# Optimization experiments

Measured on AMD Instinct MI355X. Metric: run time of the kernel, lower is better.

## Reference

```python
import jax, jax.numpy as jnp
import numpy as np

DIM = 512
EPS = 1e-8
LN_EPS = 1e-5


def _layernorm(x, g, b):
    mu = jnp.mean(x, axis=-1, keepdims=True)
    var = jnp.mean(jnp.square(x - mu), axis=-1, keepdims=True)
    return (x - mu) * jax.lax.rsqrt(var + LN_EPS) * g + b


def setup_inputs() -> dict:
    key = jax.random.key(0)
    ks = jax.random.split(key, 8)
    b, i, j, d = 8, 2048, 2048, DIM
    s = 1.0 / np.sqrt(d)
    return {
        "inputs": jax.random.normal(ks[0], (b, i, d), dtype=jnp.float32),
        "context": jax.random.normal(ks[1], (b, j, d), dtype=jnp.float32),
        "g_in": jnp.ones((d,), jnp.float32),
        "b_in": jnp.zeros((d,), jnp.float32),
        "g_ctx": jnp.ones((d,), jnp.float32),
        "b_ctx": jnp.zeros((d,), jnp.float32),
        "Wq": jax.random.uniform(ks[2], (d, d), jnp.float32, -s, s),
        "bq": jnp.zeros((d,), jnp.float32),
        "Wk": jax.random.uniform(ks[3], (d, d), jnp.float32, -s, s),
        "bk": jnp.zeros((d,), jnp.float32),
        "Wv": jax.random.uniform(ks[4], (d, d), jnp.float32, -s, s),
        "bv": jnp.zeros((d,), jnp.float32),
    }


def reference(inputs, context, g_in, b_in, g_ctx, b_ctx, Wq, bq, Wk, bk, Wv, bv):
    scale = DIM ** (-0.5)
    x = _layernorm(inputs, g_in, b_in)
    c = _layernorm(context, g_ctx, b_ctx)
    q = x @ Wq + bq          # [b,i,d]
    k = c @ Wk + bk          # [b,j,d]
    v = c @ Wv + bv          # [b,j,d]
    dots = jnp.einsum('bid,bjd->bij', q, k) * scale
    # NOTE: non-standard softmax over the QUERY axis (dim=1), then eps shift
    attn = jax.nn.softmax(dots, axis=1) + EPS
    # second renormalization over the KEY axis (dim=2)
    mean_attn = attn / (jnp.sum(attn, axis=2, keepdims=True) + EPS)
    updates = jnp.einsum('bjd,bij->bid', v, mean_attn)
    return updates
```

## Files before the change

kernel.cpp:

```cpp
#include <hip/hip_runtime.h>
#include <hip/hip_bf16.h>
#include <math.h>

#define EPSF 1e-8f
#define LN_EPSF 1e-5f
#define SCALE_QK 0.04419417382415922f

typedef unsigned short ushort_t;
typedef __bf16 bhalf;
typedef bhalf bhalf8 __attribute__((ext_vector_type(8)));
typedef float f32x4 __attribute__((ext_vector_type(4)));

__device__ __forceinline__ float b2f(ushort_t u) {
    return __uint_as_float((unsigned)u << 16);
}
__device__ __forceinline__ ushort_t f2b(float f) {
    unsigned x = __float_as_uint(f);
    return (ushort_t)((x + 0x7fffu + ((x >> 16) & 1u)) >> 16);
}
__device__ __forceinline__ unsigned pk2(float lo, float hi) {
    return (unsigned)f2b(lo) | ((unsigned)f2b(hi) << 16);
}
__device__ __forceinline__ void gload16(const ushort_t* g, ushort_t* l) {
    __builtin_amdgcn_global_load_lds(
        (const __attribute__((address_space(1))) unsigned int*)g,
        (__attribute__((address_space(3))) unsigned int*)l, 16, 0, 0);
}

__global__ __launch_bounds__(256) void mv_bias_kernel(
    const float* __restrict__ Wq, const float* __restrict__ Wk,
    const float* __restrict__ bq, const float* __restrict__ bk,
    float* __restrict__ wqbk, float* __restrict__ wkbq, float* __restrict__ cc)
{
    __shared__ float ls[4];
    const int y = blockIdx.y;
    const int t = threadIdx.x;
    if (y == 2) {
        if (blockIdx.x != 0) return;
        float s = bq[t] * bk[t] + bq[t + 256] * bk[t + 256];
#pragma unroll
        for (int off = 32; off > 0; off >>= 1) s += __shfl_down(s, off, 64);
        int lane = t & 63, w = t >> 6;
        if (lane == 0) ls[w] = s;
        __syncthreads();
        if (t == 0) cc[0] = ls[0] + ls[1] + ls[2] + ls[3];
        return;
    }
    const float* W = y ? Wk : Wq;
    const float* v = y ? bq : bk;
    float* o = y ? wkbq : wqbk;
    const int row = blockIdx.x * 16 + (t >> 4);
    const int l = t & 15;
    const float* wr = W + (size_t)row * 512 + l * 32;
    const float* vr = v + l * 32;
    float s = 0.f;
#pragma unroll
    for (int c = 0; c < 32; ++c) s += wr[c] * vr[c];
#pragma unroll
    for (int off = 8; off > 0; off >>= 1) s += __shfl_down(s, off, 16);
    if (l == 0) o[row] = s;
}

__global__ __launch_bounds__(256) void ln_apply_kernel(
    const float* __restrict__ X1, const float* __restrict__ X2,
    const float* __restrict__ g1, const float* __restrict__ b1,
    const float* __restrict__ g2, const float* __restrict__ b2,
    const float* __restrict__ wb1, const float* __restrict__ wb2,
    ushort_t* __restrict__ O1, ushort_t* __restrict__ O2,
    float* __restrict__ T1, float* __restrict__ T2)
{
    const bool sec = blockIdx.y != 0;
    const float* X = sec ? X2 : X1;
    const float* g = sec ? g2 : g1;
    const float* b = sec ? b2 : b1;
    const float* wb = sec ? wb2 : wb1;
    ushort_t* O = sec ? O2 : O1;
    float* T = sec ? T2 : T1;
    const size_t base = (size_t)blockIdx.x * 512;
    const int t = threadIdx.x;
    float2 x = ((const float2*)(X + base))[t];
    float s = x.x + x.y;
    float q = fmaf(x.x, x.x, x.y * x.y);
#pragma unroll
    for (int off = 32; off > 0; off >>= 1) {
        s += __shfl_down(s, off, 64);
        q += __shfl_down(q, off, 64);
    }
    __shared__ float ls[4], lq[4], mv[2], ld[4];
    int lane = t & 63, w = t >> 6;
    if (lane == 0) { ls[w] = s; lq[w] = q; }
    __syncthreads();
    if (t == 0) {
        float st = ls[0] + ls[1] + ls[2] + ls[3];
        float qt = lq[0] + lq[1] + lq[2] + lq[3];
        float mu = st * (1.0f / 512.0f);
        float var = qt * (1.0f / 512.0f) - mu * mu;
        mv[0] = mu;
        mv[1] = rsqrtf(var + LN_EPSF);
    }
    __syncthreads();
    const float mu = mv[0], rstd = mv[1];
    float2 gg = ((const float2*)g)[t];
    float2 bb = ((const float2*)b)[t];
    float2 ww = ((const float2*)wb)[t];
    float o0 = (x.x - mu) * rstd * gg.x + bb.x;
    float o1 = (x.y - mu) * rstd * gg.y + bb.y;
    ((unsigned*)O)[blockIdx.x * 256 + t] = pk2(o0, o1);
    float d = o0 * ww.x + o1 * ww.y;
#pragma unroll
    for (int off = 32; off > 0; off >>= 1) d += __shfl_down(d, off, 64);
    if (lane == 0) ld[w] = d;
    __syncthreads();
    if (t == 0) T[blockIdx.x] = ld[0] + ld[1] + ld[2] + ld[3];
}

__global__ __launch_bounds__(256) void wprep_kernel(
    const float* __restrict__ Wq, const float* __restrict__ Wk,
    const float* __restrict__ Wv,
    ushort_t* __restrict__ Wqb, ushort_t* __restrict__ Wkb,
    ushort_t* __restrict__ WvT)
{
    const int z = blockIdx.z;
    if (z < 2) {
        const float* W = z ? Wk : Wq;
        ushort_t* T = z ? Wkb : Wqb;
        size_t idx = ((size_t)(blockIdx.y * 16 + blockIdx.x)) * 1024 + threadIdx.x * 4;
        float4 f = *(const float4*)(W + idx);
        uint2 u;
        u.x = pk2(f.x, f.y);
        u.y = pk2(f.z, f.w);
        *(uint2*)(T + idx) = u;
        return;
    }
    __shared__ float tile[32][33];
    int tx = threadIdx.x & 31, ty = threadIdx.x >> 5;
    int r0 = blockIdx.y * 32, c0 = blockIdx.x * 32;
#pragma unroll
    for (int p = 0; p < 4; ++p)
        tile[ty + p * 8][tx] = Wv[(size_t)(r0 + ty + p * 8) * 512 + c0 + tx];
    __syncthreads();
#pragma unroll
    for (int p = 0; p < 4; ++p)
        WvT[(size_t)(c0 + ty + p * 8) * 512 + r0 + tx] = f2b(tile[tx][ty + p * 8]);
}

__global__ __launch_bounds__(256) void colrecip_kernel(
    const float* __restrict__ cs, float* __restrict__ cr,
    ushort_t* __restrict__ crs)
{
    int t = blockIdx.x * 256 + threadIdx.x;
    float r = 1.0f / cs[t];
    cr[t] = r;
    crs[t] = f2b(r);
}

template <int MODE>
__global__ __launch_bounds__(256) void mfma_gemm_kernel(
    const ushort_t* __restrict__ A, const ushort_t* __restrict__ B,
    void* __restrict__ Cout,
    const float* __restrict__ bias,
    const float* __restrict__ t1,
    const float* __restrict__ t2,
    const float* __restrict__ cc,
    float* __restrict__ colsum,
    const float* __restrict__ crcol,
    const ushort_t* __restrict__ crs,
    int K, int N, size_t strideA, size_t strideB, size_t strideC,
    float scale)
{
    __shared__ __align__(16) ushort_t As[128 * 64];
    __shared__ __align__(16) ushort_t Bs[128 * 64];
    __shared__ __align__(16) ushort_t crs_lds[(MODE == 2) ? 2048 : 8];
    const int tid = threadIdx.x;
    const ushort_t* Ab = A + strideA * blockIdx.z;
    const ushort_t* Bb = B + strideB * blockIdx.z;
    const int m0 = blockIdx.y * 128;
    const int n0 = blockIdx.x * 128;
    const int wave = tid >> 6;
    const int lane = tid & 63;
    const int fm = lane & 15;
    const int fq = lane >> 4;
    const int fq4 = fq * 4;
    const int fm7 = fm & 7;
    const int wm = (wave >> 1) * 64;
    const int wn = (wave & 1) * 64;

    const int lrow = lane >> 3;
    const int lchunk = lane & 7;
    const int scs = lchunk ^ lrow;

    const ushort_t* aSrc[4]; const ushort_t* bSrc[4];
    ushort_t* aDst[4]; ushort_t* bDst[4];
#pragma unroll
    for (int p = 0; p < 4; ++p) {
        int row = wave * 32 + p * 8 + lrow;
        aSrc[p] = Ab + (size_t)(m0 + row) * K + scs * 8;
        bSrc[p] = Bb + (size_t)(n0 + row) * K + scs * 8;
        aDst[p] = As + (wave * 32 + p * 8) * 64 + lane * 8;
        bDst[p] = Bs + (wave * 32 + p * 8) * 64 + lane * 8;
    }

    if (MODE == 2) {
        uint4 c4 = *(const uint4*)(crs + (size_t)blockIdx.z * 2048 + tid * 8);
        *(uint4*)&crs_lds[tid * 8] = c4;
    }

    const int cBase = fq ^ fm7;
    const ushort_t* aFrag[4]; const ushort_t* bFrag[4];
#pragma unroll
    for (int t = 0; t < 4; ++t) {
        aFrag[t] = As + (wm + t * 16 + fm) * 64;
        bFrag[t] = Bs + (wn + t * 16 + fm) * 64;
    }

    f32x4 acc[4][4];
    f32x4 sacc[4];
#pragma unroll
    for (int i = 0; i < 4; ++i) {
        sacc[i] = (f32x4){0.f, 0.f, 0.f, 0.f};
#pragma unroll
        for (int j = 0; j < 4; ++j) acc[i][j] = (f32x4){0.f, 0.f, 0.f, 0.f};
    }

    for (int k0 = 0; k0 < K; k0 += 64) {
        __syncthreads();
#pragma unroll
        for (int p = 0; p < 4; ++p) {
            gload16(aSrc[p] + k0, aDst[p]);
            gload16(bSrc[p] + k0, bDst[p]);
        }
        __syncthreads();
#pragma unroll
        for (int s = 0; s < 2; ++s) {
            const int off = ((cBase ^ (s << 2)) << 3);
            bhalf8 af[4], bf[4];
#pragma unroll
            for (int t = 0; t < 4; ++t) {
                af[t] = *(const bhalf8*)(aFrag[t] + off);
                bf[t] = *(const bhalf8*)(bFrag[t] + off);
            }
#pragma unroll
            for (int i = 0; i < 4; ++i)
#pragma unroll
                for (int j = 0; j < 4; ++j)
                    acc[i][j] = __builtin_amdgcn_mfma_f32_16x16x32_bf16(
                        bf[j], af[i], acc[i][j], 0, 0, 0);
            if (MODE == 2) {
                bhalf8 bc = *(const bhalf8*)&crs_lds[k0 + (s << 5) + (fq << 3)];
#pragma unroll
                for (int i = 0; i < 4; ++i)
                    sacc[i] = __builtin_amdgcn_mfma_f32_16x16x32_bf16(
                        bc, af[i], sacc[i], 0, 0, 0);
            }
        }
    }

    if (MODE == 2) {
        float* C = (float*)Cout + strideC * blockIdx.z;
#pragma unroll
        for (int ti = 0; ti < 4; ++ti) {
            const int row = m0 + wm + ti * 16 + fm;
            const float rs = 1.0f / (sacc[ti][0] + 2.049e-5f);
            float* Cr = C + (size_t)row * N + n0 + wn + fq4;
#pragma unroll
            for (int tj = 0; tj < 4; ++tj) {
                f32x4 v;
#pragma unroll
                for (int r = 0; r < 4; ++r) v[r] = acc[ti][tj][r] * rs;
                *(f32x4*)(Cr + tj * 16) = v;
            }
        }
    } else if (MODE == 1) {
        ushort_t* C = (ushort_t*)Cout + strideC * blockIdx.z;
        const float cv = cc[0];
        f32x4 t2c[4];
#pragma unroll
        for (int tj = 0; tj < 4; ++tj) {
            float4 tv = *(const float4*)(t2 + (size_t)blockIdx.z * 2048 +
                                         n0 + wn + tj * 16 + fq4);
            t2c[tj][0] = tv.x + cv;
            t2c[tj][1] = tv.y + cv;
            t2c[tj][2] = tv.z + cv;
            t2c[tj][3] = tv.w + cv;
        }
        float psum[4][4];
#pragma unroll
        for (int tj = 0; tj < 4; ++tj)
#pragma unroll
            for (int r = 0; r < 4; ++r) psum[tj][r] = 0.f;
#pragma unroll
        for (int ti = 0; ti < 4; ++ti) {
            const int row = m0 + wm + ti * 16 + fm;
            const float t1v = t1[(size_t)blockIdx.z * 2048 + row];
            ushort_t* Cr = C + (size_t)row * N + n0 + wn + fq4;
#pragma unroll
            for (int tj = 0; tj < 4; ++tj) {
                ushort_t h0 = f2b(__expf((acc[ti][tj][0] + t1v + t2c[tj][0]) * scale));
                ushort_t h1 = f2b(__expf((acc[ti][tj][1] + t1v + t2c[tj][1]) * scale));
                ushort_t h2 = f2b(__expf((acc[ti][tj][2] + t1v + t2c[tj][2]) * scale));
                ushort_t h3 = f2b(__expf((acc[ti][tj][3] + t1v + t2c[tj][3]) * scale));
                uint2 u;
                u.x = (unsigned)h0 | ((unsigned)h1 << 16);
                u.y = (unsigned)h2 | ((unsigned)h3 << 16);
                *(uint2*)(Cr + tj * 16) = u;
                psum[tj][0] += b2f(h0);
                psum[tj][1] += b2f(h1);
                psum[tj][2] += b2f(h2);
                psum[tj][3] += b2f(h3);
            }
        }
#pragma unroll
        for (int tj = 0; tj < 4; ++tj)
#pragma unroll
            for (int r = 0; r < 4; ++r) {
                float v = psum[tj][r];
                v += __shfl_xor(v, 1, 64);
                v += __shfl_xor(v, 2, 64);
                v += __shfl_xor(v, 4, 64);
                v += __shfl_xor(v, 8, 64);
                psum[tj][r] = v;
            }
        float* colpart = (float*)&As[0];
        __syncthreads();
        if (tid < 128) colpart[tid] = 0.f;
        __syncthreads();
        if (fm == 0) {
#pragma unroll
            for (int tj = 0; tj < 4; ++tj)
#pragma unroll
                for (int r = 0; r < 4; ++r)
                    atomicAdd(&colpart[wn + tj * 16 + fq4 + r], psum[tj][r]);
        }
        __syncthreads();
        if (tid < 128)
            atomicAdd(&colsum[(size_t)blockIdx.z * 2048 + n0 + tid], colpart[tid]);
    } else if (MODE == 3) {
        ushort_t* C = (ushort_t*)Cout + strideC * blockIdx.z;
        f32x4 crv[4];
#pragma unroll
        for (int tj = 0; tj < 4; ++tj) {
            float4 cq = *(const float4*)(crcol + (size_t)blockIdx.z * 2048 +
                                         n0 + wn + tj * 16 + fq4);
            crv[tj][0] = cq.x; crv[tj][1] = cq.y;
            crv[tj][2] = cq.z; crv[tj][3] = cq.w;
        }
#pragma unroll
        for (int ti = 0; ti < 4; ++ti) {
            const int row = m0 + wm + ti * 16 + fm;
            const float bvv = bias[row];
            ushort_t* Cr = C + (size_t)row * N + n0 + wn + fq4;
#pragma unroll
            for (int tj = 0; tj < 4; ++tj) {
                uint2 u;
                u.x = pk2((acc[ti][tj][0] + bvv) * crv[tj][0],
                          (acc[ti][tj][1] + bvv) * crv[tj][1]);
                u.y = pk2((acc[ti][tj][2] + bvv) * crv[tj][2],
                          (acc[ti][tj][3] + bvv) * crv[tj][3]);
                *(uint2*)(Cr + tj * 16) = u;
            }
        }
    } else {
        ushort_t* C = (ushort_t*)Cout + strideC * blockIdx.z;
#pragma unroll
        for (int ti = 0; ti < 4; ++ti) {
            const int row = m0 + wm + ti * 16 + fm;
            ushort_t* Cr = C + (size_t)row * N + n0 + wn + fq4;
#pragma unroll
            for (int tj = 0; tj < 4; ++tj) {
                uint2 u;
                u.x = pk2(acc[ti][tj][0], acc[ti][tj][1]);
                u.y = pk2(acc[ti][tj][2], acc[ti][tj][3]);
                *(uint2*)(Cr + tj * 16) = u;
            }
        }
    }
}

extern "C" void kernel_launch(void* const* d_in, const int* in_sizes, int n_in,
                              void* d_out, int out_size, void* d_ws, size_t ws_size,
                              hipStream_t stream)
{
    const float* inputs  = (const float*)d_in[0];
    const float* context = (const float*)d_in[1];
    const float* g_in    = (const float*)d_in[2];
    const float* b_in    = (const float*)d_in[3];
    const float* g_ctx   = (const float*)d_in[4];
    const float* b_ctx   = (const float*)d_in[5];
    const float* Wq      = (const float*)d_in[6];
    const float* bq      = (const float*)d_in[7];
    const float* Wk      = (const float*)d_in[8];
    const float* bk      = (const float*)d_in[9];
    const float* Wv      = (const float*)d_in[10];
    const float* bv      = (const float*)d_in[11];
    float* out = (float*)d_out;

    const size_t QKV  = 8ull * 2048 * 512;
    const size_t WSZ  = 512ull * 512;
    const size_t DOTS = 8ull * 2048 * 2048;

    ushort_t* xln   = (ushort_t*)d_ws;
    ushort_t* cln   = xln + QKV;
    ushort_t* Wqb   = cln + QKV;
    ushort_t* Wkb   = Wqb + WSZ;
    ushort_t* WvT   = Wkb + WSZ;
    ushort_t* Mb    = WvT + WSZ;
    ushort_t* KM    = Mb + WSZ;
    ushort_t* vTs   = KM + QKV;
    ushort_t* edots = vTs + QKV;
    ushort_t* crs   = edots + DOTS;
    float* fbase    = (float*)(crs + 16384);
    float* colsum   = fbase;
    float* colrecip = colsum + 16384;
    float* t1       = colrecip + 16384;
    float* t2       = t1 + 16384;
    float* wqbk     = t2 + 16384;
    float* wkbq     = wqbk + 512;
    float* cc       = wkbq + 512;
    size_t need_bytes = (4 * QKV + 4 * WSZ + DOTS + 16384) * 2
                      + (4 * 16384 + 1024 + 1) * 4;
    if (ws_size < need_bytes) return;

    hipMemsetAsync(colsum, 0, 16384 * sizeof(float), stream);

    mv_bias_kernel<<<dim3(32, 3), 256, 0, stream>>>(Wq, Wk, bq, bk, wqbk, wkbq, cc);

    ln_apply_kernel<<<dim3(16384, 2), 256, 0, stream>>>(
        inputs, context, g_in, b_in, g_ctx, b_ctx, wqbk, wkbq, xln, cln, t1, t2);

    wprep_kernel<<<dim3(16, 16, 3), 256, 0, stream>>>(Wq, Wk, Wv, Wqb, Wkb, WvT);

    mfma_gemm_kernel<0><<<dim3(4, 4, 1), 256, 0, stream>>>(
        Wqb, Wkb, Mb, nullptr, nullptr, nullptr, nullptr, nullptr, nullptr, nullptr,
        512, 512, 0, 0, 0, 1.f);

    mfma_gemm_kernel<0><<<dim3(4, 128, 1), 256, 0, stream>>>(
        cln, Mb, KM, nullptr, nullptr, nullptr, nullptr, nullptr, nullptr, nullptr,
        512, 512, 0, 0, 0, 1.f);

    mfma_gemm_kernel<1><<<dim3(16, 16, 8), 256, 0, stream>>>(
        xln, KM, edots, nullptr, t1, t2, cc, colsum, nullptr, nullptr,
        512, 2048, (size_t)2048 * 512, (size_t)2048 * 512, (size_t)2048 * 2048,
        SCALE_QK);

    colrecip_kernel<<<64, 256, 0, stream>>>(colsum, colrecip, crs);

    mfma_gemm_kernel<3><<<dim3(16, 4, 8), 256, 0, stream>>>(
        WvT, cln, vTs, bv, nullptr, nullptr, nullptr, nullptr, colrecip, nullptr,
        512, 2048, 0, (size_t)2048 * 512, (size_t)512 * 2048, 1.f);

    mfma_gemm_kernel<2><<<dim3(4, 16, 8), 256, 0, stream>>>(
        edots, vTs, out, nullptr, nullptr, nullptr, nullptr, nullptr, nullptr, crs,
        2048, 512, (size_t)2048 * 2048, (size_t)512 * 2048, (size_t)2048 * 512,
        1.f);
}
```

Measured before the change: 320.9 us.

## Double-buffer LDS tiles in MFMA GEMM to overlap loads with compute

Splits the shared-memory A/B tiles into two buffers and restructures the K loop so the next tile's global-to-LDS loads are issued before computing on the current tile. This drops one of the two barriers per iteration and hides global load latency behind MFMA work. The cost is double the LDS footprint (64KB for A/B), which may lower occupancy, and there is a risk that the single barrier does not fully order the async LDS loads.

Result: slower. 335.1 us (+4.4%).

```diff
diff --git a/kernel.cpp b/kernel.cpp
--- a/kernel.cpp
+++ b/kernel.cpp
@@ -168,8 +168,10 @@
     int K, int N, size_t strideA, size_t strideB, size_t strideC,
     float scale)
 {
-    __shared__ __align__(16) ushort_t As[128 * 64];
-    __shared__ __align__(16) ushort_t Bs[128 * 64];
+    __shared__ __align__(16) ushort_t As0[128 * 64];
+    __shared__ __align__(16) ushort_t As1[128 * 64];
+    __shared__ __align__(16) ushort_t Bs0[128 * 64];
+    __shared__ __align__(16) ushort_t Bs1[128 * 64];
     __shared__ __align__(16) ushort_t crs_lds[(MODE == 2) ? 2048 : 8];
     const int tid = threadIdx.x;
     const ushort_t* Ab = A + strideA * blockIdx.z;
@@ -190,15 +192,13 @@
     const int scs = lchunk ^ lrow;
 
     const ushort_t* aSrc[4]; const ushort_t* bSrc[4];
-    ushort_t* aDst[4]; ushort_t* bDst[4];
 #pragma unroll
     for (int p = 0; p < 4; ++p) {
         int row = wave * 32 + p * 8 + lrow;
         aSrc[p] = Ab + (size_t)(m0 + row) * K + scs * 8;
         bSrc[p] = Bb + (size_t)(n0 + row) * K + scs * 8;
-        aDst[p] = As + (wave * 32 + p * 8) * 64 + lane * 8;
-        bDst[p] = Bs + (wave * 32 + p * 8) * 64 + lane * 8;
-    }
+    }
+    const int dOff = wave * 2048 + lane * 8;
 
     if (MODE == 2) {
         uint4 c4 = *(const uint4*)(crs + (size_t)blockIdx.z * 2048 + tid * 8);
@@ -206,11 +206,11 @@
     }
 
     const int cBase = fq ^ fm7;
-    const ushort_t* aFrag[4]; const ushort_t* bFrag[4];
+    int fragA[4], fragB[4];
 #pragma unroll
     for (int t = 0; t < 4; ++t) {
-        aFrag[t] = As + (wm + t * 16 + fm) * 64;
-        bFrag[t] = Bs + (wn + t * 16 + fm) * 64;
+        fragA[t] = (wm + t * 16 + fm) * 64;
+        fragB[t] = (wn + t * 16 + fm) * 64;
     }
 
     f32x4 acc[4][4];
@@ -222,29 +222,29 @@
         for (int j = 0; j < 4; ++j) acc[i][j] = (f32x4){0.f, 0.f, 0.f, 0.f};
     }
 
-    for (int k0 = 0; k0 < K; k0 += 64) {
-        __syncthreads();
+    auto stage = [&](ushort_t* Ad, ushort_t* Bd, int k0) {
 #pragma unroll
         for (int p = 0; p < 4; ++p) {
-            gload16(aSrc[p] + k0, aDst[p]);
-            gload16(bSrc[p] + k0, bDst[p]);
-        }
-        __syncthreads();
+            gload16(aSrc[p] + k0, Ad + dOff + p * 512);
+            gload16(bSrc[p] + k0, Bd + dOff + p * 512);
+        }
+    };
+    auto compute = [&](const ushort_t* Asb, const ushort_t* Bsb, int k0) {
 #pragma unroll
         for (int s = 0; s < 2; ++s) {
             const int off = ((cBase ^ (s << 2)) << 3);
-            bhalf8 af[4], bf[4];
-#pragma unroll
-            for (int t = 0; t < 4; ++t) {
-                af[t] = *(const bhalf8*)(aFrag[t] + off);
-                bf[t] = *(const bhalf8*)(bFrag[t] + off);
+            bhalf8 af[4], bfr[4];
+#pragma unroll
+            for (int u = 0; u < 4; ++u) {
+                af[u]  = *(const bhalf8*)(Asb + fragA[u] + off);
+                bfr[u] = *(const bhalf8*)(Bsb + fragB[u] + off);
             }
 #pragma unroll
             for (int i = 0; i < 4; ++i)
 #pragma unroll
                 for (int j = 0; j < 4; ++j)
                     acc[i][j] = __builtin_amdgcn_mfma_f32_16x16x32_bf16(
-                        bf[j], af[i], acc[i][j], 0, 0, 0);
+                        bfr[j], af[i], acc[i][j], 0, 0, 0);
             if (MODE == 2) {
                 bhalf8 bc = *(const bhalf8*)&crs_lds[k0 + (s << 5) + (fq << 3)];
 #pragma unroll
@@ -253,6 +253,28 @@
                         bc, af[i], sacc[i], 0, 0, 0);
             }
         }
+    };
+
+    const int nk = K >> 6;
+    stage(As0, Bs0, 0);
+    __syncthreads();
+    int t = 0;
+    for (; t + 2 <= nk - 1; t += 2) {
+        stage(As1, Bs1, (t + 1) << 6);
+        compute(As0, Bs0, t << 6);
+        __syncthreads();
+        stage(As0, Bs0, (t + 2) << 6);
+        compute(As1, Bs1, (t + 1) << 6);
+        __syncthreads();
+    }
+    if (t < nk - 1) {
+        stage(As1, Bs1, (t + 1) << 6);
+        compute(As0, Bs0, t << 6);
+        __syncthreads();
+        ++t;
+        compute(As1, Bs1, t << 6);
+    } else {
+        compute(As0, Bs0, t << 6);
     }
 
     if (MODE == 2) {
@@ -320,7 +342,7 @@
                 v += __shfl_xor(v, 8, 64);
                 psum[tj][r] = v;
             }
-        float* colpart = (float*)&As[0];
+        float* colpart = (float*)&As0[0];
         __syncthreads();
         if (tid < 128) colpart[tid] = 0.f;
         __syncthreads();
```
